# Kernel tuning notes

Hardware: AMD Instinct MI355X
Metric: run time of the kernel (lower is better)

The kernel has to match this reference:

```python
import jax, jax.numpy as jnp
import numpy as np

S, B, D, E2 = 2048, 32, 1024, 1024  # src_len, batch, dec_hid_dim, 2*enc_hid_dim


def setup_inputs() -> dict:
    key = jax.random.key(0)
    k1, k2, k3, k4, k5 = jax.random.split(key, 5)
    scale = 1.0 / np.sqrt(D)
    return {
        "dec_prev_hidden": jax.random.normal(k1, (B, D), dtype=jnp.float32),
        "enc_outputs": jax.random.normal(k2, (S, B, E2), dtype=jnp.float32),
        "Wb": jax.random.normal(k3, (D, D), dtype=jnp.float32) * scale,
        "Wc": jax.random.normal(k4, (D, E2), dtype=jnp.float32) * scale,
        "Wa": jax.random.normal(k5, (D,), dtype=jnp.float32) * scale,
    }


def reference(dec_prev_hidden, enc_outputs, Wb, Wc, Wa):
    # weighted_s_t_1: [B, D] broadcast over seq axis; weighted_H: [S, B, D]
    weighted_s = jnp.einsum('bd,ed->be', dec_prev_hidden, Wb)          # [B, D]
    weighted_H = jnp.einsum('sbe,de->sbd', enc_outputs, Wc)            # [S, B, D]
    score = jnp.einsum('sbd,d->sb', jnp.tanh(weighted_H + weighted_s), Wa)  # [S, B]
    # torch F.softmax with no dim on a 3-D tensor -> dim=0 (seq axis)
    attn = jax.nn.softmax(score, axis=0)                               # [S, B]
    # bmm([B,1,S], [B,S,2E]) -> [B,1,2E], then permute -> [1,B,2E]
    context = jnp.einsum('sb,sbe->be', attn, enc_outputs)              # [B, 2E]
    return context[None, :, :]                                         # [1, B, 2E]
```

## Files before the change

### kernel.cpp

```cpp
#include <hip/hip_runtime.h>
#include <hip/hip_bf16.h>
#include <stdint.h>

#define S_LEN 2048
#define BATCH 32
#define MROWS (S_LEN*BATCH)

typedef __attribute__((ext_vector_type(8))) short bf16x8;
typedef __attribute__((ext_vector_type(4))) float f32x4;
typedef unsigned short ushort_t;

__device__ inline unsigned int pk2bf(float a, float b) {
  float2 t; t.x = a; t.y = b;
  __hip_bfloat162 h = __float22bfloat162_rn(t);
  union { __hip_bfloat162 h; unsigned int u; } c; c.h = h;
  return c.u;
}

__device__ inline float bflo(unsigned int u) { return __uint_as_float(u << 16); }
__device__ inline float bfhi(unsigned int u) { return __uint_as_float(u & 0xffff0000u); }

__device__ inline void gload_lds16(const void* g, void* l) {
  __builtin_amdgcn_global_load_lds(
      (const __attribute__((address_space(1))) unsigned int*)g,
      (__attribute__((address_space(3))) unsigned int*)l, 16, 0, 0);
}

__device__ inline float fast_tanh(float x) {
  float e = __expf(2.0f * x);
  return 1.0f - 2.0f / (e + 1.0f);
}

__global__ __launch_bounds__(256) void prep_conv_kernel(
    const float* __restrict__ dec, const float* __restrict__ Wb,
    const float* __restrict__ Wc, const float* __restrict__ enc,
    ushort_t* __restrict__ encBf, ushort_t* __restrict__ WcBf,
    float* __restrict__ wsum)
{
  const int t = threadIdx.x;
  const int bid = blockIdx.x;
  if (bid < 2048) {
    const size_t base = (size_t)bid * 4096;
    for (int it = 0; it < 16; ++it) {
      const size_t i = base + it * 256 + t;
      const float4* p = (const float4*)enc + i * 2;
      float4 a = p[0], b = p[1];
      uint4 w;
      w.x = pk2bf(a.x, a.y); w.y = pk2bf(a.z, a.w);
      w.z = pk2bf(b.x, b.y); w.w = pk2bf(b.z, b.w);
      ((uint4*)encBf)[i] = w;
    }
  } else if (bid < 2112) {
    const int base = (bid - 2048) * 16384;
    for (int i = 0; i < 16; ++i) {
      int idx = base + i * 1024 + t * 4;
      float4 v = *(const float4*)(Wc + idx);
      uint2 w; w.x = pk2bf(v.x, v.y); w.y = pk2bf(v.z, v.w);
      *(uint2*)(WcBf + idx) = w;
    }
  } else {
    const int j = bid - 2112;
    __shared__ float sdec[32][65];
    __shared__ float swb[32][65];
    const int b = t & 31, nl = t >> 5;
    float acc0 = 0.f, acc1 = 0.f, acc2 = 0.f, acc3 = 0.f;
    for (int c = 0; c < 16; ++c) {
      __syncthreads();
      for (int idx = t; idx < 2048; idx += 256) {
        int rr = idx >> 6, dd = idx & 63;
        sdec[rr][dd] = dec[rr * 1024 + c * 64 + dd];
        swb[rr][dd]  = Wb[(size_t)(j * 32 + rr) * 1024 + c * 64 + dd];
      }
      __syncthreads();
      #pragma unroll 8
      for (int dd = 0; dd < 64; ++dd) {
        float dv = sdec[b][dd];
        acc0 += dv * swb[nl][dd];
        acc1 += dv * swb[nl + 8][dd];
        acc2 += dv * swb[nl + 16][dd];
        acc3 += dv * swb[nl + 24][dd];
      }
    }
    wsum[b * 1024 + j * 32 + nl]      = acc0;
    wsum[b * 1024 + j * 32 + nl + 8]  = acc1;
    wsum[b * 1024 + j * 32 + nl + 16] = acc2;
    wsum[b * 1024 + j * 32 + nl + 24] = acc3;
  }
}

__global__ __launch_bounds__(512, 2) void score_kernel(
    const ushort_t* __restrict__ encBf, const ushort_t* __restrict__ WcBf,
    const float* __restrict__ wsum, const float* __restrict__ Wa,
    float* __restrict__ expS, float* __restrict__ gSumP)
{
  __shared__ ushort_t Ab[2][128][64];
  __shared__ ushort_t Bb[2][256][64];
  __shared__ float scorep[128];

  const int tid = threadIdx.x;
  const int lane = tid & 63;
  const int l15 = lane & 15, q = lane >> 4;
  const int wid = tid >> 6;
  const int wr = wid >> 2, wc = wid & 3;
  const size_t rowBase = (size_t)blockIdx.x * 128;

  if (tid < 128) scorep[tid] = 0.f;

  const int ar0 = tid >> 3, ac0 = tid & 7;
  const int aSwz = (ac0 ^ (ar0 & 7)) * 8;
  const ushort_t* aS0 = encBf + (rowBase + ar0) * 1024 + aSwz;
  const ushort_t* aS1 = aS0 + (size_t)64 * 1024;
  const int aD0 = tid * 8, aD1 = (tid + 512) * 8;

  int bSrcOff[4], bD[4];
  #pragma unroll
  for (int k = 0; k < 4; ++k) {
    const int s = k * 512 + tid;
    const int r = s >> 3, c = s & 7;
    bSrcOff[k] = r * 1024 + ((c ^ (r & 7)) * 8);
    bD[k] = s * 8;
  }

  f32x4 acc[4][4];
  #pragma unroll
  for (int m = 0; m < 4; ++m)
    #pragma unroll
    for (int n = 0; n < 4; ++n) { f32x4 z = {0.f,0.f,0.f,0.f}; acc[m][n] = z; }

  {
    ushort_t* ab = &Ab[0][0][0];
    ushort_t* bb = &Bb[0][0][0];
    gload_lds16(aS0, ab + aD0);
    gload_lds16(aS1, ab + aD1);
    #pragma unroll
    for (int k = 0; k < 4; ++k)
      gload_lds16(WcBf + bSrcOff[k], bb + bD[k]);
  }
  __syncthreads();

  for (int s = 0; s < 64; ++s) {
    const int cur = s & 1;
    if (s < 63) {
      const int s2 = s + 1;
      const int ko = (s2 & 15) * 64;
      ushort_t* ab = &Ab[cur ^ 1][0][0];
      ushort_t* bb = &Bb[cur ^ 1][0][0];
      gload_lds16(aS0 + ko, ab + aD0);
      gload_lds16(aS1 + ko, ab + aD1);
      const ushort_t* bsrc = WcBf + (size_t)(s2 >> 4) * 262144 + ko;
      #pragma unroll
      for (int k = 0; k < 4; ++k)
        gload_lds16(bsrc + bSrcOff[k], bb + bD[k]);
    }

    #pragma unroll
    for (int kk = 0; kk < 2; ++kk) {
      bf16x8 af[4], bv[4];
      #pragma unroll
      for (int m = 0; m < 4; ++m) {
        const int row = wr * 64 + m * 16 + l15;
        const int ch = (kk * 4 + q) ^ (row & 7);
        af[m] = *(const bf16x8*)&Ab[cur][row][ch * 8];
      }
      #pragma unroll
      for (int n = 0; n < 4; ++n) {
        const int row = wc * 64 + n * 16 + l15;
        const int ch = (kk * 4 + q) ^ (row & 7);
        bv[n] = *(const bf16x8*)&Bb[cur][row][ch * 8];
      }
      #pragma unroll
      for (int m = 0; m < 4; ++m)
        #pragma unroll
        for (int n = 0; n < 4; ++n)
          acc[m][n] = __builtin_amdgcn_mfma_f32_16x16x32_bf16(
              af[m], bv[n], acc[m][n], 0, 0, 0);
    }

    if ((s & 15) == 15) {
      const int nb = s >> 4;
      #pragma unroll
      for (int m = 0; m < 4; ++m) {
        #pragma unroll
        for (int i = 0; i < 4; ++i) {
          const int rowl = wr * 64 + m * 16 + q * 4 + i;
          const int bb2 = rowl & 31;
          float v = 0.f;
          #pragma unroll
          for (int n = 0; n < 4; ++n) {
            const int col = nb * 256 + wc * 64 + n * 16 + l15;
            float x = acc[m][n][i] + wsum[bb2 * 1024 + col];
            v += fast_tanh(x) * Wa[col];
          }
          v += __shfl_xor(v, 1); v += __shfl_xor(v, 2);
          v += __shfl_xor(v, 4); v += __shfl_xor(v, 8);
          if (l15 == 0) atomicAdd(&scorep[rowl], v);
        }
      }
      #pragma unroll
      for (int m = 0; m < 4; ++m)
        #pragma unroll
        for (int n = 0; n < 4; ++n) { f32x4 z = {0.f,0.f,0.f,0.f}; acc[m][n] = z; }
    }
    __syncthreads();
  }

  if (tid < 128) {
    float e = __expf(scorep[tid]);
    expS[rowBase + tid] = e;
    scorep[tid] = e;
  }
  __syncthreads();
  if (tid < 32) {
    float v = scorep[tid] + scorep[tid + 32] + scorep[tid + 64] + scorep[tid + 96];
    gSumP[tid * 512 + blockIdx.x] = v;
  }
}

__global__ __launch_bounds__(256) void ctx_kernel(
    const ushort_t* __restrict__ encBf, const float* __restrict__ expS,
    const float* __restrict__ gSumP, float* __restrict__ out)
{
  const int b = blockIdx.x & 31, sc = blockIdx.x >> 5;
  const int t = threadIdx.x;
  __shared__ float red[256];
  red[t] = gSumP[b * 512 + t] + gSumP[b * 512 + 256 + t];
  __syncthreads();
  #pragma unroll
  for (int o = 128; o > 0; o >>= 1) {
    if (t < o) red[t] += red[t + o];
    __syncthreads();
  }
  const float inv = 1.0f / red[0];

  float a0 = 0.f, a1 = 0.f, a2 = 0.f, a3 = 0.f;
  const int e0 = t * 4;
  #pragma unroll 4
  for (int si = 0; si < 128; ++si) {
    const int s = sc * 128 + si;
    const float a = expS[s * 32 + b];
    uint2 w = *(const uint2*)(encBf + ((size_t)s * 32 + b) * 1024 + e0);
    a0 += a * bflo(w.x); a1 += a * bfhi(w.x);
    a2 += a * bflo(w.y); a3 += a * bfhi(w.y);
  }
  float* op = out + b * 1024 + e0;
  atomicAdd(op + 0, a0 * inv); atomicAdd(op + 1, a1 * inv);
  atomicAdd(op + 2, a2 * inv); atomicAdd(op + 3, a3 * inv);
}

extern "C" void kernel_launch(void* const* d_in, const int* in_sizes, int n_in,
                              void* d_out, int out_size, void* d_ws, size_t ws_size,
                              hipStream_t stream) {
  const float* dec = (const float*)d_in[0];
  const float* enc = (const float*)d_in[1];
  const float* Wb  = (const float*)d_in[2];
  const float* Wc  = (const float*)d_in[3];
  const float* Wa  = (const float*)d_in[4];
  float* out = (float*)d_out;
  (void)in_sizes; (void)n_in; (void)ws_size;

  char* ws = (char*)d_ws;
  ushort_t* encBf = (ushort_t*)ws;
  ushort_t* WcBf  = (ushort_t*)(ws + 134217728);
  float*    wsum  = (float*)(ws + 134217728 + 2097152);
  float*    expS  = (float*)(ws + 134217728 + 2097152 + 131072);
  float*    gSumP = (float*)(ws + 134217728 + 2097152 + 131072 + 262144);

  hipMemsetAsync(out, 0, (size_t)out_size * sizeof(float), stream);
  prep_conv_kernel<<<2144, 256, 0, stream>>>(dec, Wb, Wc, enc, encBf, WcBf, wsum);
  score_kernel<<<512, 512, 0, stream>>>(encBf, WcBf, wsum, Wa, expS, gSumP);
  ctx_kernel<<<512, 256, 0, stream>>>(encBf, expS, gSumP, out);
}
```

Measured before the change: 444.4 us.

## Deepen A-tile prefetch pipeline and replace ctx atomics with two-pass reduction

```diff
diff --git a/kernel.cpp b/kernel.cpp
--- a/kernel.cpp
+++ b/kernel.cpp
@@ -88,38 +88,49 @@
   }
 }
 
-__global__ __launch_bounds__(512, 2) void score_kernel(
+__global__ __launch_bounds__(512, 1) void score_kernel(
     const ushort_t* __restrict__ encBf, const ushort_t* __restrict__ WcBf,
     const float* __restrict__ wsum, const float* __restrict__ Wa,
     float* __restrict__ expS, float* __restrict__ gSumP)
 {
-  __shared__ ushort_t Ab[2][128][64];
+  __shared__ ushort_t Ab[4][128][64];
   __shared__ ushort_t Bb[2][256][64];
   __shared__ float scorep[128];
 
   const int tid = threadIdx.x;
   const int lane = tid & 63;
   const int l15 = lane & 15, q = lane >> 4;
+  const int r7 = l15 & 7;
   const int wid = tid >> 6;
   const int wr = wid >> 2, wc = wid & 3;
   const size_t rowBase = (size_t)blockIdx.x * 128;
 
   if (tid < 128) scorep[tid] = 0.f;
 
+  ushort_t* const aB = &Ab[0][0][0];
+  ushort_t* const bB = &Bb[0][0][0];
+
   const int ar0 = tid >> 3, ac0 = tid & 7;
-  const int aSwz = (ac0 ^ (ar0 & 7)) * 8;
-  const ushort_t* aS0 = encBf + (rowBase + ar0) * 1024 + aSwz;
+  const ushort_t* aS0 = encBf + (rowBase + ar0) * 1024 + ((ac0 ^ (ar0 & 7)) * 8);
   const ushort_t* aS1 = aS0 + (size_t)64 * 1024;
   const int aD0 = tid * 8, aD1 = (tid + 512) * 8;
 
-  int bSrcOff[4], bD[4];
+  int bOff[4], bDst[4];
   #pragma unroll
   for (int k = 0; k < 4; ++k) {
     const int s = k * 512 + tid;
     const int r = s >> 3, c = s & 7;
-    bSrcOff[k] = r * 1024 + ((c ^ (r & 7)) * 8);
-    bD[k] = s * 8;
-  }
+    bOff[k] = r * 1024 + ((c ^ (r & 7)) * 8);
+    bDst[k] = s * 8;
+  }
+
+  int aRow[4], bRow[4];
+  #pragma unroll
+  for (int m = 0; m < 4; ++m) aRow[m] = (wr * 64 + m * 16 + l15) * 64;
+  #pragma unroll
+  for (int n = 0; n < 4; ++n) bRow[n] = (wc * 64 + n * 16 + l15) * 64;
+  const int ch0 = (q ^ r7) * 8;
+  const int ch1 = ((4 + q) ^ r7) * 8;
 
   f32x4 acc[4][4];
   #pragma unroll
@@ -127,47 +138,44 @@
     #pragma unroll
     for (int n = 0; n < 4; ++n) { f32x4 z = {0.f,0.f,0.f,0.f}; acc[m][n] = z; }
 
-  {
-    ushort_t* ab = &Ab[0][0][0];
-    ushort_t* bb = &Bb[0][0][0];
-    gload_lds16(aS0, ab + aD0);
-    gload_lds16(aS1, ab + aD1);
-    #pragma unroll
-    for (int k = 0; k < 4; ++k)
-      gload_lds16(WcBf + bSrcOff[k], bb + bD[k]);
-  }
-  __syncthreads();
-
-  for (int s = 0; s < 64; ++s) {
-    const int cur = s & 1;
-    if (s < 63) {
-      const int s2 = s + 1;
-      const int ko = (s2 & 15) * 64;
-      ushort_t* ab = &Ab[cur ^ 1][0][0];
-      ushort_t* bb = &Bb[cur ^ 1][0][0];
-      gload_lds16(aS0 + ko, ab + aD0);
-      gload_lds16(aS1 + ko, ab + aD1);
-      const ushort_t* bsrc = WcBf + (size_t)(s2 >> 4) * 262144 + ko;
+  gload_lds16(aS0, aB + aD0);
+  gload_lds16(aS1, aB + aD1);
+  #pragma unroll
+  for (int k = 0; k < 4; ++k)
+    gload_lds16(WcBf + bOff[k], bB + bDst[k]);
+  gload_lds16(aS0 + 64,  aB + 8192 + aD0);
+  gload_lds16(aS1 + 64,  aB + 8192 + aD1);
+  gload_lds16(aS0 + 128, aB + 16384 + aD0);
+  gload_lds16(aS1 + 128, aB + 16384 + aD1);
+
+  for (int t = 0; t < 64; ++t) {
+    {
+      const int jb = (t + 1) & 63;
+      const ushort_t* bsrc = WcBf + (size_t)(jb >> 4) * 262144 + (jb & 15) * 64;
+      ushort_t* bd = bB + ((t + 1) & 1) * 16384;
       #pragma unroll
       for (int k = 0; k < 4; ++k)
-        gload_lds16(bsrc + bSrcOff[k], bb + bD[k]);
-    }
-
+        gload_lds16(bsrc + bOff[k], bd + bDst[k]);
+      const int ja = t + 3;
+      const int ko = (ja & 15) * 64;
+      ushort_t* ad = aB + (ja & 3) * 8192;
+      gload_lds16(aS0 + ko, ad + aD0);
+      gload_lds16(aS1 + ko, ad + aD1);
+    }
+
+    asm volatile("s_waitcnt vmcnt(8)" ::: "memory");
+    __builtin_amdgcn_s_barrier();
+
+    const ushort_t* ab = aB + (t & 3) * 8192;
+    const ushort_t* bb = bB + (t & 1) * 16384;
     #pragma unroll
     for (int kk = 0; kk < 2; ++kk) {
+      const int cho = kk ? ch1 : ch0;
       bf16x8 af[4], bv[4];
       #pragma unroll
-      for (int m = 0; m < 4; ++m) {
-        const int row = wr * 64 + m * 16 + l15;
-        const int ch = (kk * 4 + q) ^ (row & 7);
-        af[m] = *(const bf16x8*)&Ab[cur][row][ch * 8];
-      }
-      #pragma unroll
-      for (int n = 0; n < 4; ++n) {
-        const int row = wc * 64 + n * 16 + l15;
-        const int ch = (kk * 4 + q) ^ (row & 7);
-        bv[n] = *(const bf16x8*)&Bb[cur][row][ch * 8];
-      }
+      for (int m = 0; m < 4; ++m) af[m] = *(const bf16x8*)(ab + aRow[m] + cho);
+      #pragma unroll
+      for (int n = 0; n < 4; ++n) bv[n] = *(const bf16x8*)(bb + bRow[n] + cho);
       #pragma unroll
       for (int m = 0; m < 4; ++m)
         #pragma unroll
@@ -176,8 +184,8 @@
               af[m], bv[n], acc[m][n], 0, 0, 0);
     }
 
-    if ((s & 15) == 15) {
-      const int nb = s >> 4;
+    if ((t & 15) == 15) {
+      const int nb = t >> 4;
       #pragma unroll
       for (int m = 0; m < 4; ++m) {
         #pragma unroll
@@ -201,9 +209,10 @@
         #pragma unroll
         for (int n = 0; n < 4; ++n) { f32x4 z = {0.f,0.f,0.f,0.f}; acc[m][n] = z; }
     }
-    __syncthreads();
-  }
-
+    __builtin_amdgcn_s_barrier();
+  }
+
+  __syncthreads();
   if (tid < 128) {
     float e = __expf(scorep[tid]);
     expS[rowBase + tid] = e;
@@ -216,22 +225,12 @@
   }
 }
 
-__global__ __launch_bounds__(256) void ctx_kernel(
+__global__ __launch_bounds__(256) void ctx_partial_kernel(
     const ushort_t* __restrict__ encBf, const float* __restrict__ expS,
-    const float* __restrict__ gSumP, float* __restrict__ out)
+    float* __restrict__ partial)
 {
   const int b = blockIdx.x & 31, sc = blockIdx.x >> 5;
   const int t = threadIdx.x;
-  __shared__ float red[256];
-  red[t] = gSumP[b * 512 + t] + gSumP[b * 512 + 256 + t];
-  __syncthreads();
-  #pragma unroll
-  for (int o = 128; o > 0; o >>= 1) {
-    if (t < o) red[t] += red[t + o];
-    __syncthreads();
-  }
-  const float inv = 1.0f / red[0];
-
   float a0 = 0.f, a1 = 0.f, a2 = 0.f, a3 = 0.f;
   const int e0 = t * 4;
   #pragma unroll 4
@@ -242,9 +241,33 @@
     a0 += a * bflo(w.x); a1 += a * bfhi(w.x);
     a2 += a * bflo(w.y); a3 += a * bfhi(w.y);
   }
-  float* op = out + b * 1024 + e0;
-  atomicAdd(op + 0, a0 * inv); atomicAdd(op + 1, a1 * inv);
-  atomicAdd(op + 2, a2 * inv); atomicAdd(op + 3, a3 * inv);
+  *(float4*)(partial + ((size_t)(sc * 32 + b)) * 1024 + e0) =
+      make_float4(a0, a1, a2, a3);
+}
+
+__global__ __launch_bounds__(256) void ctx_reduce_kernel(
+    const float* __restrict__ partial, const float* __restrict__ gSumP,
+    float* __restrict__ out)
+{
+  const int b = blockIdx.x, t = threadIdx.x;
+  __shared__ float red[256];
+  red[t] = gSumP[b * 512 + t] + gSumP[b * 512 + 256 + t];
+  __syncthreads();
+  #pragma unroll
+  for (int o = 128; o > 0; o >>= 1) {
+    if (t < o) red[t] += red[t + o];
+    __syncthreads();
+  }
+  const float inv = 1.0f / red[0];
+
+  float4 acc = make_float4(0.f, 0.f, 0.f, 0.f);
+  #pragma unroll
+  for (int p = 0; p < 16; ++p) {
+    float4 v = *(const float4*)(partial + ((size_t)(p * 32 + b)) * 1024 + t * 4);
+    acc.x += v.x; acc.y += v.y; acc.z += v.z; acc.w += v.w;
+  }
+  acc.x *= inv; acc.y *= inv; acc.z *= inv; acc.w *= inv;
+  *(float4*)(out + (size_t)b * 1024 + t * 4) = acc;
 }
 
 extern "C" void kernel_launch(void* const* d_in, const int* in_sizes, int n_in,
@@ -256,7 +279,7 @@
   const float* Wc  = (const float*)d_in[3];
   const float* Wa  = (const float*)d_in[4];
   float* out = (float*)d_out;
-  (void)in_sizes; (void)n_in; (void)ws_size;
+  (void)in_sizes; (void)n_in; (void)ws_size; (void)out_size;
 
   char* ws = (char*)d_ws;
   ushort_t* encBf = (ushort_t*)ws;
@@ -264,9 +287,10 @@
   float*    wsum  = (float*)(ws + 134217728 + 2097152);
   float*    expS  = (float*)(ws + 134217728 + 2097152 + 131072);
   float*    gSumP = (float*)(ws + 134217728 + 2097152 + 131072 + 262144);
-
-  hipMemsetAsync(out, 0, (size_t)out_size * sizeof(float), stream);
+  float*  partial = (float*)(ws + 134217728 + 2097152 + 131072 + 262144 + 65536);
+
   prep_conv_kernel<<<2144, 256, 0, stream>>>(dec, Wb, Wc, enc, encBf, WcBf, wsum);
   score_kernel<<<512, 512, 0, stream>>>(encBf, WcBf, wsum, Wa, expS, gSumP);
-  ctx_kernel<<<512, 256, 0, stream>>>(encBf, expS, gSumP, out);
-}
+  ctx_partial_kernel<<<512, 256, 0, stream>>>(encBf, expS, partial);
+  ctx_reduce_kernel<<<32, 256, 0, stream>>>(partial, gSumP, out);
+}
```

Result: faster. 435.6 us (-2.0%).

## Split score GEMM across N blocks and move softmax sum into ctx kernel

Applied to the files above, without the earlier changes.

```diff
diff --git a/kernel.cpp b/kernel.cpp
--- a/kernel.cpp
+++ b/kernel.cpp
@@ -88,38 +88,48 @@
   }
 }
 
-__global__ __launch_bounds__(512, 2) void score_kernel(
+__global__ __launch_bounds__(256, 4) void score_kernel(
     const ushort_t* __restrict__ encBf, const ushort_t* __restrict__ WcBf,
     const float* __restrict__ wsum, const float* __restrict__ Wa,
-    float* __restrict__ expS, float* __restrict__ gSumP)
+    float* __restrict__ scoreP8)
 {
-  __shared__ ushort_t Ab[2][128][64];
-  __shared__ ushort_t Bb[2][256][64];
+  __shared__ ushort_t Ab[128][64];
+  __shared__ ushort_t Bb[128][64];
   __shared__ float scorep[128];
 
   const int tid = threadIdx.x;
   const int lane = tid & 63;
   const int l15 = lane & 15, q = lane >> 4;
+  const int r7 = l15 & 7;
   const int wid = tid >> 6;
-  const int wr = wid >> 2, wc = wid & 3;
-  const size_t rowBase = (size_t)blockIdx.x * 128;
+  const int wr = wid >> 1, wc = wid & 1;
+  const int bid = blockIdx.x;
+  const int mi = bid & 15, nblk = (bid >> 4) & 7, mg = bid >> 7;
+  const size_t rowBase = (size_t)(mg * 16 + mi) * 128;
 
   if (tid < 128) scorep[tid] = 0.f;
 
-  const int ar0 = tid >> 3, ac0 = tid & 7;
-  const int aSwz = (ac0 ^ (ar0 & 7)) * 8;
-  const ushort_t* aS0 = encBf + (rowBase + ar0) * 1024 + aSwz;
-  const ushort_t* aS1 = aS0 + (size_t)64 * 1024;
-  const int aD0 = tid * 8, aD1 = (tid + 512) * 8;
-
-  int bSrcOff[4], bD[4];
+  int aOff[4], bOff[4], dOff[4];
   #pragma unroll
   for (int k = 0; k < 4; ++k) {
-    const int s = k * 512 + tid;
+    const int s = k * 256 + tid;
     const int r = s >> 3, c = s & 7;
-    bSrcOff[k] = r * 1024 + ((c ^ (r & 7)) * 8);
-    bD[k] = s * 8;
-  }
+    const int swz = (c ^ (r & 7)) * 8;
+    aOff[k] = (int)(r * 1024 + swz);
+    bOff[k] = (int)((nblk * 128 + r) * 1024 + swz);
+    dOff[k] = s * 8;
+  }
+  const ushort_t* aBase = encBf + rowBase * 1024;
+  ushort_t* const aL = &Ab[0][0];
+  ushort_t* const bL = &Bb[0][0];
+
+  int aRow[4], bRow[4];
+  #pragma unroll
+  for (int m = 0; m < 4; ++m) aRow[m] = (wr * 64 + m * 16 + l15) * 64;
+  #pragma unroll
+  for (int n = 0; n < 4; ++n) bRow[n] = (wc * 64 + n * 16 + l15) * 64;
+  const int ch0 = (q ^ r7) * 8;
+  const int ch1 = ((4 + q) ^ r7) * 8;
 
   f32x4 acc[4][4];
   #pragma unroll
@@ -127,47 +137,23 @@
     #pragma unroll
     for (int n = 0; n < 4; ++n) { f32x4 z = {0.f,0.f,0.f,0.f}; acc[m][n] = z; }
 
-  {
-    ushort_t* ab = &Ab[0][0][0];
-    ushort_t* bb = &Bb[0][0][0];
-    gload_lds16(aS0, ab + aD0);
-    gload_lds16(aS1, ab + aD1);
-    #pragma unroll
-    for (int k = 0; k < 4; ++k)
-      gload_lds16(WcBf + bSrcOff[k], bb + bD[k]);
-  }
-  __syncthreads();
-
-  for (int s = 0; s < 64; ++s) {
-    const int cur = s & 1;
-    if (s < 63) {
-      const int s2 = s + 1;
-      const int ko = (s2 & 15) * 64;
-      ushort_t* ab = &Ab[cur ^ 1][0][0];
-      ushort_t* bb = &Bb[cur ^ 1][0][0];
-      gload_lds16(aS0 + ko, ab + aD0);
-      gload_lds16(aS1 + ko, ab + aD1);
-      const ushort_t* bsrc = WcBf + (size_t)(s2 >> 4) * 262144 + ko;
-      #pragma unroll
-      for (int k = 0; k < 4; ++k)
-        gload_lds16(bsrc + bSrcOff[k], bb + bD[k]);
-    }
+  for (int kt = 0; kt < 16; ++kt) {
+    const int ko = kt * 64;
+    #pragma unroll
+    for (int k = 0; k < 4; ++k) {
+      gload_lds16(aBase + ko + aOff[k], aL + dOff[k]);
+      gload_lds16(WcBf + ko + bOff[k], bL + dOff[k]);
+    }
+    __syncthreads();
 
     #pragma unroll
     for (int kk = 0; kk < 2; ++kk) {
+      const int cho = kk ? ch1 : ch0;
       bf16x8 af[4], bv[4];
       #pragma unroll
-      for (int m = 0; m < 4; ++m) {
-        const int row = wr * 64 + m * 16 + l15;
-        const int ch = (kk * 4 + q) ^ (row & 7);
-        af[m] = *(const bf16x8*)&Ab[cur][row][ch * 8];
-      }
-      #pragma unroll
-      for (int n = 0; n < 4; ++n) {
-        const int row = wc * 64 + n * 16 + l15;
-        const int ch = (kk * 4 + q) ^ (row & 7);
-        bv[n] = *(const bf16x8*)&Bb[cur][row][ch * 8];
-      }
+      for (int m = 0; m < 4; ++m) af[m] = *(const bf16x8*)(aL + aRow[m] + cho);
+      #pragma unroll
+      for (int n = 0; n < 4; ++n) bv[n] = *(const bf16x8*)(bL + bRow[n] + cho);
       #pragma unroll
       for (int m = 0; m < 4; ++m)
         #pragma unroll
@@ -175,55 +161,52 @@
           acc[m][n] = __builtin_amdgcn_mfma_f32_16x16x32_bf16(
               af[m], bv[n], acc[m][n], 0, 0, 0);
     }
-
-    if ((s & 15) == 15) {
-      const int nb = s >> 4;
-      #pragma unroll
-      for (int m = 0; m < 4; ++m) {
-        #pragma unroll
-        for (int i = 0; i < 4; ++i) {
-          const int rowl = wr * 64 + m * 16 + q * 4 + i;
-          const int bb2 = rowl & 31;
-          float v = 0.f;
-          #pragma unroll
-          for (int n = 0; n < 4; ++n) {
-            const int col = nb * 256 + wc * 64 + n * 16 + l15;
-            float x = acc[m][n][i] + wsum[bb2 * 1024 + col];
-            v += fast_tanh(x) * Wa[col];
-          }
-          v += __shfl_xor(v, 1); v += __shfl_xor(v, 2);
-          v += __shfl_xor(v, 4); v += __shfl_xor(v, 8);
-          if (l15 == 0) atomicAdd(&scorep[rowl], v);
-        }
+    __syncthreads();
+  }
+
+  #pragma unroll
+  for (int m = 0; m < 4; ++m) {
+    #pragma unroll
+    for (int i = 0; i < 4; ++i) {
+      const int rowl = wr * 64 + m * 16 + q * 4 + i;
+      const int bb2 = rowl & 31;
+      float v = 0.f;
+      #pragma unroll
+      for (int n = 0; n < 4; ++n) {
+        const int col = nblk * 128 + wc * 64 + n * 16 + l15;
+        float x = acc[m][n][i] + wsum[bb2 * 1024 + col];
+        v += fast_tanh(x) * Wa[col];
       }
-      #pragma unroll
-      for (int m = 0; m < 4; ++m)
-        #pragma unroll
-        for (int n = 0; n < 4; ++n) { f32x4 z = {0.f,0.f,0.f,0.f}; acc[m][n] = z; }
-    }
-    __syncthreads();
-  }
-
-  if (tid < 128) {
-    float e = __expf(scorep[tid]);
-    expS[rowBase + tid] = e;
-    scorep[tid] = e;
+      v += __shfl_xor(v, 1); v += __shfl_xor(v, 2);
+      v += __shfl_xor(v, 4); v += __shfl_xor(v, 8);
+      if (l15 == 0) atomicAdd(&scorep[rowl], v);
+    }
   }
   __syncthreads();
-  if (tid < 32) {
-    float v = scorep[tid] + scorep[tid + 32] + scorep[tid + 64] + scorep[tid + 96];
-    gSumP[tid * 512 + blockIdx.x] = v;
-  }
+  if (tid < 128) scoreP8[(rowBase + tid) * 8 + nblk] = scorep[tid];
 }
 
 __global__ __launch_bounds__(256) void ctx_kernel(
-    const ushort_t* __restrict__ encBf, const float* __restrict__ expS,
-    const float* __restrict__ gSumP, float* __restrict__ out)
+    const ushort_t* __restrict__ encBf, const float* __restrict__ scoreP8,
+    float* __restrict__ out)
 {
   const int b = blockIdx.x & 31, sc = blockIdx.x >> 5;
   const int t = threadIdx.x;
+  __shared__ float eCh[128];
   __shared__ float red[256];
-  red[t] = gSumP[b * 512 + t] + gSumP[b * 512 + 256 + t];
+
+  const int chunk0 = sc * 128;
+  float ssum = 0.f;
+  for (int s = t; s < S_LEN; s += 256) {
+    const float4* p = (const float4*)(scoreP8 + ((size_t)s * 32 + b) * 8);
+    float4 u = p[0], v = p[1];
+    float scv = ((u.x + u.y) + (u.z + u.w)) + ((v.x + v.y) + (v.z + v.w));
+    float e = __expf(scv);
+    ssum += e;
+    const int d = s - chunk0;
+    if ((unsigned)d < 128u) eCh[d] = e;
+  }
+  red[t] = ssum;
   __syncthreads();
   #pragma unroll
   for (int o = 128; o > 0; o >>= 1) {
@@ -236,8 +219,8 @@
   const int e0 = t * 4;
   #pragma unroll 4
   for (int si = 0; si < 128; ++si) {
-    const int s = sc * 128 + si;
-    const float a = expS[s * 32 + b];
+    const int s = chunk0 + si;
+    const float a = eCh[si];
     uint2 w = *(const uint2*)(encBf + ((size_t)s * 32 + b) * 1024 + e0);
     a0 += a * bflo(w.x); a1 += a * bfhi(w.x);
     a2 += a * bflo(w.y); a3 += a * bfhi(w.y);
@@ -259,14 +242,13 @@
   (void)in_sizes; (void)n_in; (void)ws_size;
 
   char* ws = (char*)d_ws;
-  ushort_t* encBf = (ushort_t*)ws;
-  ushort_t* WcBf  = (ushort_t*)(ws + 134217728);
-  float*    wsum  = (float*)(ws + 134217728 + 2097152);
-  float*    expS  = (float*)(ws + 134217728 + 2097152 + 131072);
-  float*    gSumP = (float*)(ws + 134217728 + 2097152 + 131072 + 262144);
+  ushort_t* encBf   = (ushort_t*)ws;
+  ushort_t* WcBf    = (ushort_t*)(ws + 134217728);
+  float*    wsum    = (float*)(ws + 134217728 + 2097152);
+  float*    scoreP8 = (float*)(ws + 134217728 + 2097152 + 131072);
 
   hipMemsetAsync(out, 0, (size_t)out_size * sizeof(float), stream);
   prep_conv_kernel<<<2144, 256, 0, stream>>>(dec, Wb, Wc, enc, encBf, WcBf, wsum);
-  score_kernel<<<512, 512, 0, stream>>>(encBf, WcBf, wsum, Wa, expS, gSumP);
-  ctx_kernel<<<512, 256, 0, stream>>>(encBf, expS, gSumP, out);
-}
+  score_kernel<<<4096, 256, 0, stream>>>(encBf, WcBf, wsum, Wa, scoreP8);
+  ctx_kernel<<<512, 256, 0, stream>>>(encBf, scoreP8, out);
+}
```

Measured after the change: 383.6 us. -13.7%, faster.
